# Performance work log

Hardware: AMD Instinct MI355X
Metric: run time of the kernel (lower is better)

Reference implementation:

```python
import jax, jax.numpy as jnp
import numpy as np

B, S, DIN = 2, 2048, 1024
H = 16
DK = 1024   # dim_key_query_all
DV = 1024   # dim_value_all
DOUT = 1024
HEAD_SIZE = DK / H  # attention_head_size (float division in source)
LN_EPS = 1e-5


def setup_inputs() -> dict:
    key = jax.random.key(0)
    ks = jax.random.split(key, 12)
    s_in = 1.0 / np.sqrt(DIN)
    s_dv = 1.0 / np.sqrt(DV)
    return {
        "hidden_states": jax.random.normal(ks[0], (B, S, DIN), jnp.float32),
        "Wq": jax.random.uniform(ks[1], (DK, DIN), jnp.float32, -s_in, s_in),
        "Wk": jax.random.uniform(ks[2], (DK, DIN), jnp.float32, -s_in, s_in),
        "Wcb": jax.random.uniform(ks[3], (H, DIN), jnp.float32, -s_in, s_in),
        "Wv": jax.random.uniform(ks[4], (DV, DIN), jnp.float32, -s_in, s_in),
        "bv": jax.random.uniform(ks[5], (DV,), jnp.float32, -s_in, s_in),
        "mixing": 0.2 * jax.random.normal(ks[6], (H, DK), jnp.float32),
        "Wd": jax.random.uniform(ks[7], (DOUT, DV), jnp.float32, -s_dv, s_dv),
        "bd": jax.random.uniform(ks[8], (DOUT,), jnp.float32, -s_dv, s_dv),
        "gamma": jnp.ones((DV,), jnp.float32),
        "beta": jnp.zeros((DV,), jnp.float32),
    }


def reference(hidden_states, Wq, Wk, Wcb, Wv, bv, mixing, Wd, bd, gamma, beta):
    x = hidden_states  # [B, S, DIN]; self-attention: from == to
    q = jnp.einsum('bsd,kd->bsk', x, Wq)  # [B,S,DK]
    k = jnp.einsum('bsd,kd->bsk', x, Wk)  # [B,S,DK]
    # scores[b,h,i,j] = sum_c q[b,i,c]*mixing[h,c]*k[b,j,c]
    scores = jnp.einsum('bic,hc,bjc->bhij', q, mixing, k)
    cb = jnp.einsum('bjd,hd->bhj', x, Wcb)  # content bias [B,H,S]
    scores = scores + cb[:, :, None, :]
    scores = scores / jnp.sqrt(jnp.asarray(HEAD_SIZE, scores.dtype))
    probs = jax.nn.softmax(scores, axis=-1)  # dropout p=0.0 -> identity
    v = jnp.einsum('bsd,vd->bsv', x, Wv) + bv  # [B,S,DV]
    v = v.reshape(B, S, H, DV // H)
    ctx = jnp.einsum('bhij,bjhv->bihv', probs, v).reshape(B, S, DV)
    out = jnp.einsum('bsv,ov->bso', ctx, Wd) + bd
    res = x + out
    mu = jnp.mean(res, axis=-1, keepdims=True)
    var = jnp.var(res, axis=-1, keepdims=True)
    out = (res - mu) * jax.lax.rsqrt(var + LN_EPS) * gamma + beta
    return (out,)
```

## Files before the change

### kernel.cpp

```cpp
#include <hip/hip_runtime.h>
#include <cstddef>
#include <cstdint>

#define B_    2
#define S_    2048
#define DIN_  1024
#define H_    16
#define DK_   1024
#define DV_   1024
#define DH_   64
#define DOUT_ 1024
#define M_    (B_ * S_)

typedef __attribute__((ext_vector_type(8)))  short short8;
typedef __attribute__((ext_vector_type(4)))  float float4v;
typedef __attribute__((ext_vector_type(16))) float float16v;
typedef _Float16 half8v __attribute__((ext_vector_type(8)));

__device__ __forceinline__ float bf16s_to_f(short s) {
  union { unsigned int u; float f; } cv;
  cv.u = ((unsigned int)(unsigned short)s) << 16;
  return cv.f;
}
__device__ __forceinline__ short f_to_bf16s(float f) {
  union { float f; unsigned int u; } cv;
  cv.f = f;
  unsigned int u = cv.u + 0x7FFFu + ((cv.u >> 16) & 1u);
  return (short)(u >> 16);
}
__device__ __forceinline__ short f_to_f16s(float f) {
  union { _Float16 h; short s; } cv;
  cv.h = (_Float16)f;
  return cv.s;
}
__device__ __forceinline__ unsigned pkrtz_u32(float a, float b) {
  union { __fp16 __attribute__((ext_vector_type(2))) h2; unsigned u; } cv;
  cv.h2 = __builtin_amdgcn_cvt_pkrtz(a, b);
  return cv.u;
}
__device__ __forceinline__ void gll16(const void* g, void* l) {
  __builtin_amdgcn_global_load_lds(
      (const __attribute__((address_space(1))) unsigned int*)g,
      (__attribute__((address_space(3))) unsigned int*)l, 16, 0, 0);
}

__global__ __launch_bounds__(256) void cast_kernel(const float* __restrict__ in,
                                                   short* __restrict__ out, int n4) {
  int i = blockIdx.x * 256 + threadIdx.x;
  if (i >= n4) return;
  float4 v = ((const float4*)in)[i];
  union { ushort4 u; short s[4]; } o;
  o.s[0] = f_to_bf16s(v.x); o.s[1] = f_to_bf16s(v.y);
  o.s[2] = f_to_bf16s(v.z); o.s[3] = f_to_bf16s(v.w);
  ((ushort4*)out)[i] = o.u;
}

__global__ __launch_bounds__(256) void cb_kernel(const float* __restrict__ x,
                                                 const float* __restrict__ Wcb,
                                                 float* __restrict__ CBs) {
  __shared__ float xs[DIN_];
  const int row = blockIdx.x;
  const int tid = threadIdx.x;
  #pragma unroll
  for (int it = 0; it < 4; ++it)
    xs[tid + it * 256] = x[(size_t)row * DIN_ + tid + it * 256];
  __syncthreads();
  const int lane = tid & 63, w = tid >> 6;
  const float SC = 0.125f * 1.44269504088896f;
  #pragma unroll
  for (int hh = 0; hh < 4; ++hh) {
    const int hidx = w * 4 + hh;
    float p = 0.f;
    for (int c = lane; c < DIN_; c += 64)
      p += xs[c] * Wcb[(size_t)hidx * DIN_ + c];
    #pragma unroll
    for (int mk = 1; mk < 64; mk <<= 1) p += __shfl_xor(p, mk);
    if (lane == 0) {
      const int bb = row / S_, ss = row % S_;
      CBs[((size_t)bb * H_ + hidx) * S_ + ss] = p * SC;
    }
  }
}

__global__ __launch_bounds__(256, 2) void gemm_nt(
    const short* __restrict__ A, const short* __restrict__ Bw,
    const float* __restrict__ bias, const float* __restrict__ resid,
    short* __restrict__ outb, float* __restrict__ outf, int mode) {
  const int KD = 1024, ND = 1024;
  __shared__ short As[64][136];
  __shared__ short Bs[64][136];
  const int tid  = threadIdx.x;
  const int lane = tid & 63;
  const int w    = tid >> 6;
  const int quad = lane >> 4;
  const int l16  = lane & 15;
  const int m0   = blockIdx.y * 64;
  const int n0   = blockIdx.x * 64;
  const int wm   = (w >> 1) * 32;
  const int wn   = (w & 1) * 32;
  const int srow = tid >> 2;
  const int sseg = (tid & 3) * 32;

  const float4v zero = {0.f, 0.f, 0.f, 0.f};
  float4v acc[2][2];
  acc[0][0] = zero; acc[0][1] = zero; acc[1][0] = zero; acc[1][1] = zero;

  for (int k0 = 0; k0 < KD; k0 += 128) {
    short8 ar[4], br[4];
    #pragma unroll
    for (int c = 0; c < 4; ++c) {
      ar[c] = *(const short8*)(A  + (size_t)(m0 + srow) * KD + k0 + sseg + c * 8);
      br[c] = *(const short8*)(Bw + (size_t)(n0 + srow) * KD + k0 + sseg + c * 8);
    }
    __syncthreads();
    #pragma unroll
    for (int c = 0; c < 4; ++c) {
      *(short8*)&As[srow][sseg + c * 8] = ar[c];
      *(short8*)&Bs[srow][sseg + c * 8] = br[c];
    }
    __syncthreads();
    #pragma unroll
    for (int ks = 0; ks < 4; ++ks) {
      short8 af0 = *(short8*)&As[wm + l16][ks * 32 + quad * 8];
      short8 af1 = *(short8*)&As[wm + 16 + l16][ks * 32 + quad * 8];
      short8 bg0 = *(short8*)&Bs[wn + l16][ks * 32 + quad * 8];
      short8 bg1 = *(short8*)&Bs[wn + 16 + l16][ks * 32 + quad * 8];
      acc[0][0] = __builtin_amdgcn_mfma_f32_16x16x32_bf16(af0, bg0, acc[0][0], 0, 0, 0);
      acc[0][1] = __builtin_amdgcn_mfma_f32_16x16x32_bf16(af0, bg1, acc[0][1], 0, 0, 0);
      acc[1][0] = __builtin_amdgcn_mfma_f32_16x16x32_bf16(af1, bg0, acc[1][0], 0, 0, 0);
      acc[1][1] = __builtin_amdgcn_mfma_f32_16x16x32_bf16(af1, bg1, acc[1][1], 0, 0, 0);
    }
  }

  #pragma unroll
  for (int mt = 0; mt < 2; ++mt)
    #pragma unroll
    for (int nt = 0; nt < 2; ++nt)
      #pragma unroll
      for (int r = 0; r < 4; ++r) {
        int row = m0 + wm + mt * 16 + quad * 4 + r;
        int col = n0 + wn + nt * 16 + l16;
        float v = acc[mt][nt][r];
        if (mode == 1 || mode == 5) v += bias[col];
        if (mode == 2)
          outf[(size_t)row * ND + col] = v + bias[col] + resid[(size_t)row * ND + col];
        else if (mode == 5) {
          int bb = row >> 11, ss = row & 2047;
          outb[((size_t)bb * DV_ + col) * S_ + ss] = f_to_f16s(v);
        } else if (mode == 4)
          outb[(size_t)row * ND + col] = f_to_f16s(v);
        else
          outb[(size_t)row * ND + col] = f_to_bf16s(v);
      }
}

__global__ __launch_bounds__(256, 2) void attn_kernel(
    const short* __restrict__ Qf, const short* __restrict__ Kf,
    const short* __restrict__ Vtf, const float* __restrict__ mixing,
    const float* __restrict__ CBs, short* __restrict__ ctxb) {
  __shared__ __align__(16) short KsF[128 * 128];
  __shared__ __align__(16) short Vt[64][136];
  __shared__ __align__(16) short mix_s[DK_];
  __shared__ float cb_s[128];

  const int tid  = threadIdx.x;
  const int lane = tid & 63;
  const int l32  = lane & 31;
  const int l1   = lane >> 5;
  const int w    = tid >> 6;

  const int F    = blockIdx.x;
  const int xcd  = F & 7, rest = F >> 3;
  const int b    = xcd >> 2;
  const int h    = (xcd & 3) * 4 + (rest & 3);
  const int i0   = (rest >> 2) * 128;

  const float SC = 0.125f * 1.44269504088896f;
  for (int c = tid; c < DK_; c += 256) {
    union { _Float16 h; short s; } cv;
    cv.h = (_Float16)(mixing[(size_t)h * DK_ + c] * SC);
    mix_s[c] = cv.s;
  }

  const int iq = i0 + w * 32 + l32;
  const short* qptr  = Qf + ((size_t)b * S_ + iq) * DK_;
  const short* kbase = Kf + (size_t)b * S_ * DK_;
  const short* vtb   = Vtf + ((size_t)b * DV_ + h * DH_) * S_;
  const float* cbp   = CBs + ((size_t)b * H_ + h) * S_;

  float16v accS[4], accO[2];
  #pragma unroll
  for (int g = 0; g < 2; ++g)
    #pragma unroll
    for (int r = 0; r < 16; ++r) accO[g][r] = 0.f;
  float m_run = -1e30f, l_run = 0.f;

  const int drow_l = lane >> 4;
  const int dp     = lane & 15;

  const int vrow = tid >> 2;
  const int vseg = (tid & 3) * 32;

  for (int j0 = 0; j0 < S_; j0 += 128) {
    short8 vreg[4];
    #pragma unroll
    for (int c = 0; c < 4; ++c)
      vreg[c] = *(const short8*)(vtb + (size_t)vrow * S_ + j0 + vseg + c * 8);
    float cbv = 0.f;
    if (tid < 128) cbv = cbp[j0 + tid];
    __syncthreads();
    #pragma unroll
    for (int c = 0; c < 4; ++c)
      *(short8*)&Vt[vrow][vseg + c * 8] = vreg[c];
    if (tid < 128) cb_s[tid] = cbv;

    #pragma unroll
    for (int f = 0; f < 4; ++f)
      #pragma unroll
      for (int r = 0; r < 16; ++r) accS[f][r] = 0.f;

    for (int kc = 0; kc < 8; ++kc) {
      half8v qraw[8];
      #pragma unroll
      for (int ks = 0; ks < 8; ++ks)
        qraw[ks] = *(const half8v*)(qptr + kc * 128 + ks * 16 + l1 * 8);
      __syncthreads();
      #pragma unroll
      for (int cc = 0; cc < 8; ++cc) {
        const int n = w * 8 + cc;
        const int r = 4 * n + drow_l;
        const int lchunk = dp ^ (r & 15);
        gll16(kbase + (size_t)(j0 + r) * DK_ + kc * 128 + lchunk * 8,
              &KsF[n * 512]);
      }
      __syncthreads();

      #pragma unroll
      for (int ks = 0; ks < 8; ++ks) {
        half8v mf = *(half8v*)&mix_s[kc * 128 + ks * 16 + l1 * 8];
        half8v qm = qraw[ks] * mf;
        const int poff = ((2 * ks + l1) ^ (l32 & 15)) * 8 + l32 * 128;
        #pragma unroll
        for (int f = 0; f < 4; ++f) {
          half8v af = *(half8v*)&KsF[f * 4096 + poff];
          accS[f] = __builtin_amdgcn_mfma_f32_32x32x16_f16(af, qm, accS[f], 0, 0, 0);
        }
      }
    }

    float tmax = -1e30f;
    #pragma unroll
    for (int f = 0; f < 4; ++f)
      #pragma unroll
      for (int q = 0; q < 4; ++q) {
        float4 cbq = *(float4*)&cb_s[f * 32 + q * 8 + l1 * 4];
        #pragma unroll
        for (int c = 0; c < 4; ++c) {
          accS[f][4 * q + c] += ((const float*)&cbq)[c];
          tmax = fmaxf(tmax, accS[f][4 * q + c]);
        }
      }
    tmax = fmaxf(tmax, __shfl_xor(tmax, 32));
    const float mnew = fmaxf(m_run, tmax);
    const float alpha = exp2f(m_run - mnew);
    float tsum = 0.f;
    #pragma unroll
    for (int f = 0; f < 4; ++f)
      #pragma unroll
      for (int r = 0; r < 16; ++r) {
        float pv = exp2f(accS[f][r] - mnew);
        accS[f][r] = pv;
        tsum += pv;
      }
    tsum += __shfl_xor(tsum, 32);
    l_run = l_run * alpha + tsum;
    m_run = mnew;
    #pragma unroll
    for (int g = 0; g < 2; ++g)
      #pragma unroll
      for (int r = 0; r < 16; ++r) accO[g][r] *= alpha;

    #pragma unroll
    for (int cpv = 0; cpv < 8; ++cpv) {
      const int t = cpv & 1, fp = cpv >> 1;
      float xo[4], yo[4], lo[4], hi[4];
      #pragma unroll
      for (int c = 0; c < 4; ++c) {
        xo[c] = __shfl_xor(accS[fp][8 * t + c], 32);
        yo[c] = __shfl_xor(accS[fp][8 * t + 4 + c], 32);
      }
      #pragma unroll
      for (int c = 0; c < 4; ++c) {
        lo[c] = l1 ? yo[c] : accS[fp][8 * t + c];
        hi[c] = l1 ? accS[fp][8 * t + 4 + c] : xo[c];
      }
      union { half8v v; unsigned u[4]; } pb;
      pb.u[0] = pkrtz_u32(lo[0], lo[1]);
      pb.u[1] = pkrtz_u32(lo[2], lo[3]);
      pb.u[2] = pkrtz_u32(hi[0], hi[1]);
      pb.u[3] = pkrtz_u32(hi[2], hi[3]);
      #pragma unroll
      for (int g = 0; g < 2; ++g) {
        half8v vf = *(half8v*)&Vt[g * 32 + l32][cpv * 16 + l1 * 8];
        accO[g] = __builtin_amdgcn_mfma_f32_32x32x16_f16(vf, pb.v, accO[g], 0, 0, 0);
      }
    }
  }

  const float rl = 1.0f / l_run;
  short* cbase = ctxb + ((size_t)b * S_ + iq) * DV_ + h * DH_;
  #pragma unroll
  for (int g = 0; g < 2; ++g)
    #pragma unroll
    for (int q = 0; q < 4; ++q) {
      const int dv = g * 32 + 8 * q + 4 * l1;
      union { ushort4 u4; short s[4]; } ov;
      #pragma unroll
      for (int r = 0; r < 4; ++r)
        ov.s[r] = f_to_bf16s(accO[g][4 * q + r] * rl);
      *(ushort4*)(cbase + dv) = ov.u4;
    }
}

__global__ __launch_bounds__(256) void ln_kernel(float* __restrict__ out,
                                                 const float* __restrict__ gamma,
                                                 const float* __restrict__ beta) {
  __shared__ float red[8];
  const int row = blockIdx.x;
  const int tid = threadIdx.x;
  float* p = out + (size_t)row * DOUT_;
  float4 v = ((const float4*)p)[tid];
  float s = v.x + v.y + v.z + v.w;
  #pragma unroll
  for (int mk = 1; mk < 64; mk <<= 1) s += __shfl_xor(s, mk);
  if ((tid & 63) == 0) red[tid >> 6] = s;
  __syncthreads();
  const float mean = (red[0] + red[1] + red[2] + red[3]) * (1.0f / 1024.0f);
  const float d0 = v.x - mean, d1 = v.y - mean, d2 = v.z - mean, d3 = v.w - mean;
  float sq = d0 * d0 + d1 * d1 + d2 * d2 + d3 * d3;
  #pragma unroll
  for (int mk = 1; mk < 64; mk <<= 1) sq += __shfl_xor(sq, mk);
  if ((tid & 63) == 0) red[4 + (tid >> 6)] = sq;
  __syncthreads();
  const float var = (red[4] + red[5] + red[6] + red[7]) * (1.0f / 1024.0f);
  const float rstd = rsqrtf(var + 1e-5f);
  float4 g = ((const float4*)gamma)[tid];
  float4 bt = ((const float4*)beta)[tid];
  float4 o;
  o.x = d0 * rstd * g.x + bt.x;
  o.y = d1 * rstd * g.y + bt.y;
  o.z = d2 * rstd * g.z + bt.z;
  o.w = d3 * rstd * g.w + bt.w;
  ((float4*)p)[tid] = o;
}

extern "C" void kernel_launch(void* const* d_in, const int* in_sizes, int n_in,
                              void* d_out, int out_size, void* d_ws, size_t ws_size,
                              hipStream_t stream) {
  (void)in_sizes; (void)n_in; (void)out_size; (void)ws_size;
  const float* x      = (const float*)d_in[0];
  const float* Wq     = (const float*)d_in[1];
  const float* Wk     = (const float*)d_in[2];
  const float* Wcb    = (const float*)d_in[3];
  const float* Wv     = (const float*)d_in[4];
  const float* bv     = (const float*)d_in[5];
  const float* mixing = (const float*)d_in[6];
  const float* Wd     = (const float*)d_in[7];
  const float* bd     = (const float*)d_in[8];
  const float* gamma  = (const float*)d_in[9];
  const float* beta   = (const float*)d_in[10];
  float* out = (float*)d_out;

  short* p = (short*)d_ws;
  short* xb   = p; p += (size_t)M_ * DIN_;
  short* Qf   = p; p += (size_t)M_ * DK_;
  short* Kf   = p; p += (size_t)M_ * DK_;
  short* Vtf  = p; p += (size_t)B_ * DV_ * S_;
  short* ctxb = p; p += (size_t)M_ * DV_;
  short* Wqb  = p; p += (size_t)DK_ * DIN_;
  short* Wkb  = p; p += (size_t)DK_ * DIN_;
  short* Wvb  = p; p += (size_t)DV_ * DIN_;
  short* Wdb  = p; p += (size_t)DOUT_ * DV_;
  float* CBs  = (float*)p;

  cast_kernel<<<dim3(M_ * DIN_ / 1024), 256, 0, stream>>>(x, xb, M_ * DIN_ / 4);
  cast_kernel<<<dim3(DK_ * DIN_ / 1024), 256, 0, stream>>>(Wq, Wqb, DK_ * DIN_ / 4);
  cast_kernel<<<dim3(DK_ * DIN_ / 1024), 256, 0, stream>>>(Wk, Wkb, DK_ * DIN_ / 4);
  cast_kernel<<<dim3(DV_ * DIN_ / 1024), 256, 0, stream>>>(Wv, Wvb, DV_ * DIN_ / 4);
  cast_kernel<<<dim3(DOUT_ * DV_ / 1024), 256, 0, stream>>>(Wd, Wdb, DOUT_ * DV_ / 4);
  cb_kernel<<<dim3(M_), 256, 0, stream>>>(x, Wcb, CBs);

  dim3 gg(DOUT_ / 64, M_ / 64);
  gemm_nt<<<gg, 256, 0, stream>>>(xb, Wqb, nullptr, nullptr, Qf, nullptr, 4);
  gemm_nt<<<gg, 256, 0, stream>>>(xb, Wkb, nullptr, nullptr, Kf, nullptr, 4);
  gemm_nt<<<gg, 256, 0, stream>>>(xb, Wvb, bv, nullptr, Vtf, nullptr, 5);

  attn_kernel<<<dim3(512), 256, 0, stream>>>(Qf, Kf, Vtf, mixing, CBs, ctxb);

  gemm_nt<<<gg, 256, 0, stream>>>(ctxb, Wdb, bd, x, nullptr, out, 2);
  ln_kernel<<<dim3(M_), 256, 0, stream>>>(out, gamma, beta);
}
```

Measured before the change: 640.9 us.

## Double-buffer K tiles in LDS with 64-wide chunks and prefetch Q

Splits the QK^T reduction over DK into 16 chunks of 64 instead of 8 chunks of 128, and stores K in two LDS buffers so the global-to-LDS load of the next chunk overlaps the MFMAs on the current one. Q fragments for the next chunk are prefetched into registers, and wave priority is raised around the MFMA block. This cuts one barrier per chunk and hides load latency, at the cost of more iterations and extra registers for the prefetched Q.

```diff
diff --git a/kernel.cpp b/kernel.cpp
--- a/kernel.cpp
+++ b/kernel.cpp
@@ -158,7 +158,7 @@
     const short* __restrict__ Qf, const short* __restrict__ Kf,
     const short* __restrict__ Vtf, const float* __restrict__ mixing,
     const float* __restrict__ CBs, short* __restrict__ ctxb) {
-  __shared__ __align__(16) short KsF[128 * 128];
+  __shared__ __align__(16) short KsF[2 * 128 * 64];
   __shared__ __align__(16) short Vt[64][136];
   __shared__ __align__(16) short mix_s[DK_];
   __shared__ float cb_s[128];
@@ -195,8 +195,8 @@
     for (int r = 0; r < 16; ++r) accO[g][r] = 0.f;
   float m_run = -1e30f, l_run = 0.f;
 
-  const int drow_l = lane >> 4;
-  const int dp     = lane & 15;
+  const int nrow = lane >> 3;
+  const int dp8  = lane & 7;
 
   const int vrow = tid >> 2;
   const int vseg = (tid & 3) * 32;
@@ -215,37 +215,58 @@
     if (tid < 128) cb_s[tid] = cbv;
 
     #pragma unroll
+    for (int cc = 0; cc < 4; ++cc) {
+      const int n = w * 4 + cc;
+      const int r = 8 * n + nrow;
+      const int lchunk = dp8 ^ (r & 7);
+      gll16(kbase + (size_t)(j0 + r) * DK_ + lchunk * 8, &KsF[n * 512]);
+    }
+    half8v qcur[4], qnext[4];
+    #pragma unroll
+    for (int ks = 0; ks < 4; ++ks) {
+      qcur[ks] = *(const half8v*)(qptr + ks * 16 + l1 * 8);
+      qnext[ks] = qcur[ks];
+    }
+
+    #pragma unroll
     for (int f = 0; f < 4; ++f)
       #pragma unroll
       for (int r = 0; r < 16; ++r) accS[f][r] = 0.f;
 
-    for (int kc = 0; kc < 8; ++kc) {
-      half8v qraw[8];
-      #pragma unroll
-      for (int ks = 0; ks < 8; ++ks)
-        qraw[ks] = *(const half8v*)(qptr + kc * 128 + ks * 16 + l1 * 8);
-      __syncthreads();
-      #pragma unroll
-      for (int cc = 0; cc < 8; ++cc) {
-        const int n = w * 8 + cc;
-        const int r = 4 * n + drow_l;
-        const int lchunk = dp ^ (r & 15);
-        gll16(kbase + (size_t)(j0 + r) * DK_ + kc * 128 + lchunk * 8,
-              &KsF[n * 512]);
-      }
-      __syncthreads();
-
-      #pragma unroll
-      for (int ks = 0; ks < 8; ++ks) {
-        half8v mf = *(half8v*)&mix_s[kc * 128 + ks * 16 + l1 * 8];
-        half8v qm = qraw[ks] * mf;
-        const int poff = ((2 * ks + l1) ^ (l32 & 15)) * 8 + l32 * 128;
+    __syncthreads();
+
+    for (int t = 0; t < 16; ++t) {
+      if (t < 15) {
+        const int nb = (t + 1) & 1;
+        #pragma unroll
+        for (int cc = 0; cc < 4; ++cc) {
+          const int n = w * 4 + cc;
+          const int r = 8 * n + nrow;
+          const int lchunk = dp8 ^ (r & 7);
+          gll16(kbase + (size_t)(j0 + r) * DK_ + (t + 1) * 64 + lchunk * 8,
+                &KsF[nb * 8192 + n * 512]);
+        }
+        #pragma unroll
+        for (int ks = 0; ks < 4; ++ks)
+          qnext[ks] = *(const half8v*)(qptr + (t + 1) * 64 + ks * 16 + l1 * 8);
+      }
+      const short* kb = &KsF[(t & 1) * 8192];
+      __builtin_amdgcn_s_setprio(1);
+      #pragma unroll
+      for (int ks = 0; ks < 4; ++ks) {
+        half8v mf = *(half8v*)&mix_s[t * 64 + ks * 16 + l1 * 8];
+        half8v qm = qcur[ks] * mf;
+        const int poff = (((2 * ks + l1) ^ (l32 & 7)) * 8) + l32 * 64;
         #pragma unroll
         for (int f = 0; f < 4; ++f) {
-          half8v af = *(half8v*)&KsF[f * 4096 + poff];
+          half8v af = *(half8v*)&kb[f * 2048 + poff];
           accS[f] = __builtin_amdgcn_mfma_f32_32x32x16_f16(af, qm, accS[f], 0, 0, 0);
         }
       }
+      __builtin_amdgcn_s_setprio(0);
+      #pragma unroll
+      for (int ks = 0; ks < 4; ++ks) qcur[ks] = qnext[ks];
+      __syncthreads();
     }
 
     float tmax = -1e30f;
```

New measurement: 642.3 us. Within noise of the previous version (+0.2%).

## Load K fragments directly from global into registers, dropping LDS staging

Applied to the files above, without the earlier changes.

The attention kernel no longer stages K tiles into shared memory with global_load_lds and two barriers per k-chunk. Each wave now reads its own K fragments straight from global memory into registers, double-buffered across ks steps, with setprio raised around the MFMA groups. This removes LDS traffic and the per-chunk block syncs, but every wave now reads the full 128-row K tile itself, so global/L2 traffic for K rises fourfold and load latency is exposed more directly.

```diff
diff --git a/kernel.cpp b/kernel.cpp
--- a/kernel.cpp
+++ b/kernel.cpp
@@ -37,11 +37,6 @@
   union { __fp16 __attribute__((ext_vector_type(2))) h2; unsigned u; } cv;
   cv.h2 = __builtin_amdgcn_cvt_pkrtz(a, b);
   return cv.u;
-}
-__device__ __forceinline__ void gll16(const void* g, void* l) {
-  __builtin_amdgcn_global_load_lds(
-      (const __attribute__((address_space(1))) unsigned int*)g,
-      (__attribute__((address_space(3))) unsigned int*)l, 16, 0, 0);
 }
 
 __global__ __launch_bounds__(256) void cast_kernel(const float* __restrict__ in,
@@ -158,7 +153,6 @@
     const short* __restrict__ Qf, const short* __restrict__ Kf,
     const short* __restrict__ Vtf, const float* __restrict__ mixing,
     const float* __restrict__ CBs, short* __restrict__ ctxb) {
-  __shared__ __align__(16) short KsF[128 * 128];
   __shared__ __align__(16) short Vt[64][136];
   __shared__ __align__(16) short mix_s[DK_];
   __shared__ float cb_s[128];
@@ -195,9 +189,6 @@
     for (int r = 0; r < 16; ++r) accO[g][r] = 0.f;
   float m_run = -1e30f, l_run = 0.f;
 
-  const int drow_l = lane >> 4;
-  const int dp     = lane & 15;
-
   const int vrow = tid >> 2;
   const int vseg = (tid & 3) * 32;
 
@@ -213,37 +204,49 @@
     for (int c = 0; c < 4; ++c)
       *(short8*)&Vt[vrow][vseg + c * 8] = vreg[c];
     if (tid < 128) cb_s[tid] = cbv;
+    __syncthreads();
 
     #pragma unroll
     for (int f = 0; f < 4; ++f)
       #pragma unroll
       for (int r = 0; r < 16; ++r) accS[f][r] = 0.f;
 
+    const short* krow = kbase + (size_t)(j0 + l32) * DK_ + l1 * 8;
+
+    half8v afA[4], afB[4];
+    #pragma unroll
+    for (int f = 0; f < 4; ++f)
+      afA[f] = *(const half8v*)(krow + (size_t)f * 32 * DK_);
+
     for (int kc = 0; kc < 8; ++kc) {
-      half8v qraw[8];
-      #pragma unroll
-      for (int ks = 0; ks < 8; ++ks)
-        qraw[ks] = *(const half8v*)(qptr + kc * 128 + ks * 16 + l1 * 8);
-      __syncthreads();
-      #pragma unroll
-      for (int cc = 0; cc < 8; ++cc) {
-        const int n = w * 8 + cc;
-        const int r = 4 * n + drow_l;
-        const int lchunk = dp ^ (r & 15);
-        gll16(kbase + (size_t)(j0 + r) * DK_ + kc * 128 + lchunk * 8,
-              &KsF[n * 512]);
-      }
-      __syncthreads();
-
+      half8v qm[8];
       #pragma unroll
       for (int ks = 0; ks < 8; ++ks) {
+        half8v qr = *(const half8v*)(qptr + kc * 128 + ks * 16 + l1 * 8);
         half8v mf = *(half8v*)&mix_s[kc * 128 + ks * 16 + l1 * 8];
-        half8v qm = qraw[ks] * mf;
-        const int poff = ((2 * ks + l1) ^ (l32 & 15)) * 8 + l32 * 128;
-        #pragma unroll
-        for (int f = 0; f < 4; ++f) {
-          half8v af = *(half8v*)&KsF[f * 4096 + poff];
-          accS[f] = __builtin_amdgcn_mfma_f32_32x32x16_f16(af, qm, accS[f], 0, 0, 0);
+        qm[ks] = qr * mf;
+      }
+      #pragma unroll
+      for (int ks = 0; ks < 8; ++ks) {
+        const int ncol = (kc * 128 + ks * 16 + 16) & 1023;
+        if ((ks & 1) == 0) {
+          #pragma unroll
+          for (int f = 0; f < 4; ++f)
+            afB[f] = *(const half8v*)(krow + (size_t)f * 32 * DK_ + ncol);
+          __builtin_amdgcn_s_setprio(1);
+          #pragma unroll
+          for (int f = 0; f < 4; ++f)
+            accS[f] = __builtin_amdgcn_mfma_f32_32x32x16_f16(afA[f], qm[ks], accS[f], 0, 0, 0);
+          __builtin_amdgcn_s_setprio(0);
+        } else {
+          #pragma unroll
+          for (int f = 0; f < 4; ++f)
+            afA[f] = *(const half8v*)(krow + (size_t)f * 32 * DK_ + ncol);
+          __builtin_amdgcn_s_setprio(1);
+          #pragma unroll
+          for (int f = 0; f < 4; ++f)
+            accS[f] = __builtin_amdgcn_mfma_f32_32x32x16_f16(afB[f], qm[ks], accS[f], 0, 0, 0);
+          __builtin_amdgcn_s_setprio(0);
         }
       }
     }
```

Measured after the change: 1.410 ms. 2.2x slower.
